# Optimization experiments

Hardware: AMD Instinct MI355X
Metric: run time of the kernel (lower is better)

Reference implementation:

```python
import jax, jax.numpy as jnp
import numpy as np

HEADS = 2
K_HOP = 2
RATIO = 0.8
NEG_SLOPE = 0.01


def seg_softmax(logits, seg, num_seg):
    # torch_geometric.utils.softmax: numerically stable segment softmax
    m = jax.ops.segment_max(logits, seg, num_segments=num_seg)
    e = jnp.exp(logits - m[seg])
    d = jax.ops.segment_sum(e, seg, num_segments=num_seg)
    return e / d[seg]


def _attention(key_value, query, seg, num_seg, Wk, W1, W2, W3):
    # Attention.forward with enable_BN=False; weights stored [in,out] so x@W == torch Linear
    a = key_value @ Wk
    h = jnp.concatenate([a, query, a - query, a * query], axis=-1)  # [N,4H]
    h = jax.nn.leaky_relu(h @ W1, NEG_SLOPE)
    h = jax.nn.leaky_relu(h @ W2, NEG_SLOPE)
    h = jax.nn.leaky_relu(h @ W3, NEG_SLOPE)  # [N,1]
    return seg_softmax(h[:, 0], seg, num_seg)[:, None]  # att_weights [N,1]


def setup_inputs():
    key = jax.random.key(0)
    ks = jax.random.split(key, 10)
    B, n, H, epg = 64, 64, 128, 2048
    N = B * n
    x = jax.random.normal(ks[0], (N, H), jnp.float32)
    src = jax.random.randint(ks[1], (B, epg), 0, n)
    dst = jax.random.randint(ks[2], (B, epg), 0, n)
    off = (jnp.arange(B) * n)[:, None]
    edge_index = jnp.stack([(src + off).reshape(-1), (dst + off).reshape(-1)], 0)
    edge_weight = jax.random.uniform(ks[3], (B * epg,), jnp.float32)
    target_x = jax.random.normal(ks[4], (B, H), jnp.float32)
    batch_ixs = jnp.repeat(jnp.arange(B), n)
    s = lambda i, sh: jax.random.normal(ks[i], sh, jnp.float32) / np.sqrt(sh[-2])
    # index 0=cluster_att, 1=query_att, 2=cluster_att2, 3=query_att2
    att_Wk = s(5, (4, H, H))
    att_W1 = s(6, (4, 4 * H, 2 * H))
    att_W2 = s(7, (4, 2 * H, H))
    att_W3 = s(8, (4, H, 1))
    lin_W = s(9, (HEADS, H, H))
    return dict(x=x, edge_index=edge_index, edge_weight=edge_weight, target_x=target_x,
                batch_ixs=batch_ixs, att_Wk=att_Wk, att_W1=att_W1, att_W2=att_W2,
                att_W3=att_W3, lin_W=lin_W)


def reference(x, edge_index, edge_weight, target_x, batch_ixs, att_Wk, att_W1, att_W2, att_W3, lin_W):
    N, H = x.shape
    B = target_x.shape[0]
    n = N // B
    # ---- gcn_norm with self loops (fill 1.0) ----
    loop = jnp.arange(N)
    row = jnp.concatenate([edge_index[0], loop])
    col = jnp.concatenate([edge_index[1], loop])
    w = jnp.concatenate([edge_weight, jnp.ones((N,), edge_weight.dtype)])
    deg = jax.ops.segment_sum(w, col, num_segments=N)
    dinv = jnp.where(deg > 0, jax.lax.rsqrt(jnp.maximum(deg, 1e-12)), 0.0)
    ew = dinv[row] * w * dinv[col]  # [L]
    # ---- k-hop propagation ----
    def hop(v):
        return jax.ops.segment_sum(v[row] * ew[:, None], col, num_segments=N)
    x_q = x
    for _ in range(K_HOP):
        x_q = hop(x_q)
    qt = target_x[batch_ixs]  # repeat_interleave by per-graph counts (sorted batch)
    # ---- multi-head edge attention (reuse_att_w=True, dropout=0 -> E identical per head) ----
    f1 = _attention(x, x_q, batch_ixs, B, att_Wk[0], att_W1[0], att_W2[0], att_W3[0])
    f2 = _attention(x, qt, batch_ixs, B, att_Wk[1], att_W1[1], att_W2[1], att_W3[1])
    E = jax.nn.leaky_relu(f1[col] + f2[row], NEG_SLOPE)  # [L,1]
    E = seg_softmax(E[:, 0], col, N)[:, None]
    x_c = jnp.zeros_like(x)
    E_g = jnp.zeros((row.shape[0], 1), x.dtype)
    agg = jax.ops.segment_sum(x[row] * E, col, num_segments=N)
    for h in range(HEADS):
        x_c = x_c + jax.nn.leaky_relu(x + agg @ lin_W[h], NEG_SLOPE)
        E_g = E_g + E
    x_c = x_c / HEADS
    E_g = E_g / HEADS
    # ---- second k-hop + cluster scoring ----
    x_q2 = x_c
    for _ in range(K_HOP):
        x_q2 = hop(x_q2)
    g1 = _attention(x_c, x_q2, batch_ixs, B, att_Wk[2], att_W1[2], att_W2[2], att_W3[2])
    g2 = _attention(x_c, qt, batch_ixs, B, att_Wk[3], att_W1[3], att_W2[3], att_W3[3])
    # stack over heads then mean == g1+g2 (same attention modules reused per head)
    cluster_score = seg_softmax((g1 + g2)[:, 0], batch_ixs, B)  # [N]
    # ---- per-graph topk (ratio) ----
    kk = int(np.ceil(RATIO * n))
    _, idx = jax.lax.top_k(cluster_score.reshape(B, n), kk)  # descending, matches PyG topk
    perm = (idx + (jnp.arange(B) * n)[:, None]).reshape(-1)  # [Nk]
    x_out = x[perm] * cluster_score[perm][:, None]
    batch_out = batch_ixs[perm]
    # ---- S^T A S (dense equivalent of SparseTensor triple product) ----
    A_d = jnp.zeros((N, N), x.dtype).at[row, col].add(ew)
    S_d = jnp.zeros((N, N), x.dtype).at[row, col].add(E_g[:, 0])
    S_p = S_d[:, perm]  # S[:, perm] -> [N, Nk]
    A2 = S_p.T @ (A_d @ S_p)  # [Nk, Nk]
    Nk = perm.shape[0]
    A2 = A2.at[jnp.arange(Nk), jnp.arange(Nk)].set(1.0)  # fill_diag(1.0)
    return x_out, A2, batch_out, perm
```

## Files before the change

### kernel.cpp

```cpp
#include <hip/hip_runtime.h>

#define KK 52
#define NKOUT 3328
#define NEG 0.01f

typedef __attribute__((ext_vector_type(8))) __bf16 bf16x8;
typedef __attribute__((ext_vector_type(16))) float floatx16;

__device__ __forceinline__ float lrelu(float v){ return v > 0.f ? v : NEG*v; }

#define SW(r, ko) ((r)*40 + ((ko) ^ ((((r)>>3)&3) << 3)))

__device__ __forceinline__ void split_store8(const float* vv, __bf16* P0, __bf16* P1, __bf16* P2, int addr){
  bf16x8 p1, p2, p3;
  #pragma unroll
  for (int j = 0; j < 8; j++){
    __bf16 b1 = (__bf16)vv[j];
    float r1 = vv[j] - (float)b1;
    __bf16 b2 = (__bf16)r1;
    float r2 = r1 - (float)b2;
    p1[j] = b1; p2[j] = b2; p3[j] = (__bf16)r2;
  }
  *(bf16x8*)(P0 + addr) = p1;
  *(bf16x8*)(P1 + addr) = p2;
  *(bf16x8*)(P2 + addr) = p3;
}

__device__ __forceinline__ void mfma6(const __bf16* A0, const __bf16* A1, const __bf16* A2,
                                      const __bf16* B0, const __bf16* B1, const __bf16* B2,
                                      int aoff, int boff, floatx16* acc){
  bf16x8 a1 = *(const bf16x8*)(A0 + aoff);
  bf16x8 a2 = *(const bf16x8*)(A1 + aoff);
  bf16x8 a3 = *(const bf16x8*)(A2 + aoff);
  bf16x8 b1 = *(const bf16x8*)(B0 + boff);
  bf16x8 b2 = *(const bf16x8*)(B1 + boff);
  bf16x8 b3 = *(const bf16x8*)(B2 + boff);
  floatx16 c = *acc;
  c = __builtin_amdgcn_mfma_f32_32x32x16_bf16(a1,b1,c,0,0,0);
  c = __builtin_amdgcn_mfma_f32_32x32x16_bf16(a1,b2,c,0,0,0);
  c = __builtin_amdgcn_mfma_f32_32x32x16_bf16(a2,b1,c,0,0,0);
  c = __builtin_amdgcn_mfma_f32_32x32x16_bf16(a1,b3,c,0,0,0);
  c = __builtin_amdgcn_mfma_f32_32x32x16_bf16(a3,b1,c,0,0,0);
  c = __builtin_amdgcn_mfma_f32_32x32x16_bf16(a2,b2,c,0,0,0);
  *acc = c;
}

__device__ __forceinline__ void g_gemm(const float* __restrict__ A0, int ldA,
                                       const float* __restrict__ W0, int ldW, int K,
                                       __bf16* pb, floatx16* oA, floatx16* oB){
  __bf16 *As0 = pb, *As1 = pb+2560, *As2 = pb+5120;
  __bf16 *Bs0 = pb+7680, *Bs1 = pb+12800, *Bs2 = pb+17920;
  int tid = threadIdx.x;
  int sar = tid >> 2, sako = (tid & 3)*8;
  int bn = tid & 127, bk = (tid >> 7)*16;
  int wv_ = tid >> 6, L = tid & 63, m = L & 31, half = L >> 5;
  int rA = 32*(wv_ & 1) + m, rB0 = (wv_ >> 1)*32 + m, rB1 = rB0 + 64;
  const float* arow = A0 + (size_t)sar*ldA;
  floatx16 accA, accB;
  #pragma unroll
  for (int i = 0; i < 16; i++){ accA[i] = 0.f; accB[i] = 0.f; }
  float ra[8], wv[16];
  {
    float4 v0 = *(const float4*)(arow + sako);
    float4 v1 = *(const float4*)(arow + sako + 4);
    ra[0]=v0.x; ra[1]=v0.y; ra[2]=v0.z; ra[3]=v0.w; ra[4]=v1.x; ra[5]=v1.y; ra[6]=v1.z; ra[7]=v1.w;
    #pragma unroll
    for (int j = 0; j < 16; j++) wv[j] = W0[(size_t)(bk + j)*ldW + bn];
  }
  for (int k0 = 0; k0 < K; k0 += 32){
    split_store8(ra, As0, As1, As2, SW(sar, sako));
    split_store8(wv,     Bs0, Bs1, Bs2, SW(bn, bk));
    split_store8(wv + 8, Bs0, Bs1, Bs2, SW(bn, bk + 8));
    __syncthreads();
    int k1 = k0 + 32;
    float ra2[8], wv2[16];
    if (k1 < K){
      float4 v0 = *(const float4*)(arow + k1 + sako);
      float4 v1 = *(const float4*)(arow + k1 + sako + 4);
      ra2[0]=v0.x; ra2[1]=v0.y; ra2[2]=v0.z; ra2[3]=v0.w; ra2[4]=v1.x; ra2[5]=v1.y; ra2[6]=v1.z; ra2[7]=v1.w;
      #pragma unroll
      for (int j = 0; j < 16; j++) wv2[j] = W0[(size_t)(k1 + bk + j)*ldW + bn];
    }
    #pragma unroll
    for (int kg = 0; kg < 2; kg++){
      int ko = kg*16 + half*8;
      mfma6(As0,As1,As2, Bs0,Bs1,Bs2, SW(rA,ko), SW(rB0,ko), &accA);
      mfma6(As0,As1,As2, Bs0,Bs1,Bs2, SW(rA,ko), SW(rB1,ko), &accB);
    }
    __syncthreads();
    if (k1 < K){
      #pragma unroll
      for (int j = 0; j < 8; j++) ra[j] = ra2[j];
      #pragma unroll
      for (int j = 0; j < 16; j++) wv[j] = wv2[j];
    }
  }
  *oA = accA; *oB = accB;
}

__device__ __forceinline__ void g_gemm64(const float* __restrict__ A0, int ldA,
                                         const float* __restrict__ W0, int ldW, int K,
                                         __bf16* pb, floatx16* oC){
  __bf16 *As0 = pb, *As1 = pb+2560, *As2 = pb+5120;
  __bf16 *Bs0 = pb+7680, *Bs1 = pb+10240, *Bs2 = pb+12800;
  int tid = threadIdx.x;
  int sar = tid >> 2, sako = (tid & 3)*8;
  int bn = tid & 63, bk = (tid >> 6)*8;
  int wv_ = tid >> 6, L = tid & 63, m = L & 31, half = L >> 5;
  int rA = 32*(wv_ & 1) + m, rB = 32*(wv_ >> 1) + m;
  const float* arow = A0 + (size_t)sar*ldA;
  floatx16 acc;
  #pragma unroll
  for (int i = 0; i < 16; i++) acc[i] = 0.f;
  float ra[8], wv[8];
  {
    float4 v0 = *(const float4*)(arow + sako);
    float4 v1 = *(const float4*)(arow + sako + 4);
    ra[0]=v0.x; ra[1]=v0.y; ra[2]=v0.z; ra[3]=v0.w; ra[4]=v1.x; ra[5]=v1.y; ra[6]=v1.z; ra[7]=v1.w;
    #pragma unroll
    for (int j = 0; j < 8; j++) wv[j] = W0[(size_t)(bk + j)*ldW + bn];
  }
  for (int k0 = 0; k0 < K; k0 += 32){
    split_store8(ra, As0, As1, As2, SW(sar, sako));
    split_store8(wv, Bs0, Bs1, Bs2, SW(bn, bk));
    __syncthreads();
    int k1 = k0 + 32;
    float ra2[8], wv2[8];
    if (k1 < K){
      float4 v0 = *(const float4*)(arow + k1 + sako);
      float4 v1 = *(const float4*)(arow + k1 + sako + 4);
      ra2[0]=v0.x; ra2[1]=v0.y; ra2[2]=v0.z; ra2[3]=v0.w; ra2[4]=v1.x; ra2[5]=v1.y; ra2[6]=v1.z; ra2[7]=v1.w;
      #pragma unroll
      for (int j = 0; j < 8; j++) wv2[j] = W0[(size_t)(k1 + bk + j)*ldW + bn];
    }
    #pragma unroll
    for (int kg = 0; kg < 2; kg++){
      int ko = kg*16 + half*8;
      mfma6(As0,As1,As2, Bs0,Bs1,Bs2, SW(rA,ko), SW(rB,ko), &acc);
    }
    __syncthreads();
    if (k1 < K){
      #pragma unroll
      for (int j = 0; j < 8; j++){ ra[j] = ra2[j]; wv[j] = wv2[j]; }
    }
  }
  *oC = acc;
}

__device__ __forceinline__ void g_gemm_h64(const float* __restrict__ arow, const float* __restrict__ qrow,
                                           const float* __restrict__ W1fz, int colbase,
                                           __bf16* pb, floatx16* oC){
  __bf16 *As0 = pb, *As1 = pb+2560, *As2 = pb+5120;
  __bf16 *Bs0 = pb+7680, *Bs1 = pb+10240, *Bs2 = pb+12800;
  int tid = threadIdx.x;
  int sar = tid >> 2, sako = (tid & 3)*8;
  int bn = tid & 63, bk = (tid >> 6)*8;
  int col = colbase + bn;
  int wv_ = tid >> 6, L = tid & 63, m = L & 31, half = L >> 5;
  int rA = 32*(wv_ & 1) + m, rB = 32*(wv_ >> 1) + m;
  auto loadA = [&](int k0, float* r){
    int seg = k0 >> 7, kl = (k0 & 127) + sako;
    if (seg == 0){
      float4 a0 = *(const float4*)(arow + kl), a1 = *(const float4*)(arow + kl + 4);
      r[0]=a0.x; r[1]=a0.y; r[2]=a0.z; r[3]=a0.w; r[4]=a1.x; r[5]=a1.y; r[6]=a1.z; r[7]=a1.w;
    } else if (seg == 1){
      float4 q0 = *(const float4*)(qrow + kl), q1 = *(const float4*)(qrow + kl + 4);
      r[0]=q0.x; r[1]=q0.y; r[2]=q0.z; r[3]=q0.w; r[4]=q1.x; r[5]=q1.y; r[6]=q1.z; r[7]=q1.w;
    } else {
      float4 a0 = *(const float4*)(arow + kl), a1 = *(const float4*)(arow + kl + 4);
      float4 q0 = *(const float4*)(qrow + kl), q1 = *(const float4*)(qrow + kl + 4);
      r[0]=a0.x*q0.x; r[1]=a0.y*q0.y; r[2]=a0.z*q0.z; r[3]=a0.w*q0.w;
      r[4]=a1.x*q1.x; r[5]=a1.y*q1.y; r[6]=a1.z*q1.z; r[7]=a1.w*q1.w;
    }
  };
  auto loadB = [&](int k0, float* r){
    #pragma unroll
    for (int j = 0; j < 8; j++) r[j] = W1fz[(size_t)(k0 + bk + j)*256 + col];
  };
  floatx16 acc;
  #pragma unroll
  for (int i = 0; i < 16; i++) acc[i] = 0.f;
  float ra[8], wv[8];
  loadA(0, ra); loadB(0, wv);
  for (int k0 = 0; k0 < 384; k0 += 32){
    split_store8(ra, As0, As1, As2, SW(sar, sako));
    split_store8(wv, Bs0, Bs1, Bs2, SW(bn, bk));
    __syncthreads();
    int k1 = k0 + 32;
    float ra2[8], wv2[8];
    if (k1 < 384){ loadA(k1, ra2); loadB(k1, wv2); }
    #pragma unroll
    for (int kg = 0; kg < 2; kg++){
      int ko = kg*16 + half*8;
      mfma6(As0,As1,As2, Bs0,Bs1,Bs2, SW(rA,ko), SW(rB,ko), &acc);
    }
    __syncthreads();
    if (k1 < 384){
      #pragma unroll
      for (int j = 0; j < 8; j++){ ra[j] = ra2[j]; wv[j] = wv2[j]; }
    }
  }
  *oC = acc;
}

__device__ __forceinline__ void c_write(floatx16 accA, floatx16 accB, float* C0, int ldC, int act){
  int tid = threadIdx.x, wv_ = tid >> 6, L = tid & 63, m = L & 31, half = L >> 5;
  int rB0 = (wv_ >> 1)*32 + m, rB1 = rB0 + 64;
  int row0 = 32*(wv_ & 1) + 4*half;
  #pragma unroll
  for (int reg = 0; reg < 16; reg++){
    int row = row0 + (reg & 3) + 8*(reg >> 2);
    float va = accA[reg], vb = accB[reg];
    if (act){ va = lrelu(va); vb = lrelu(vb); }
    C0[(size_t)row*ldC + rB0] = va;
    C0[(size_t)row*ldC + rB1] = vb;
  }
}

__device__ __forceinline__ void c_write64(floatx16 acc, float* C0, int ldC, int act){
  int tid = threadIdx.x, wv_ = tid >> 6, L = tid & 63, m = L & 31, half = L >> 5;
  int col = 32*(wv_ >> 1) + m;
  int row0 = 32*(wv_ & 1) + 4*half;
  #pragma unroll
  for (int reg = 0; reg < 16; reg++){
    int row = row0 + (reg & 3) + 8*(reg >> 2);
    float v = acc[reg];
    if (act) v = lrelu(v);
    C0[(size_t)row*ldC + col] = v;
  }
}

__device__ __forceinline__ void hop2_run(const float* A, const float* VfullL,
                                         const float* srcG, float* dstG,
                                         float* Vt, float* Tt){
  int tid = threadIdx.x;
  int tc = (tid & 31)*2, tf = (tid >> 5)*4;
  for (int f0 = 0; f0 < 128; f0 += 32){
    if (!VfullL){
      for (int o = tid; o < 2048; o += 256){
        int r = o >> 5, f = o & 31;
        Vt[o] = srcG[r*128 + f0 + f];
      }
      __syncthreads();
    }
    float a00,a01,a02,a03,a10,a11,a12,a13;
    a00=a01=a02=a03=a10=a11=a12=a13=0.f;
    for (int r = 0; r < 64; r++){
      float x0 = A[r*64 + tc], x1 = A[r*64 + tc + 1];
      float4 v4 = VfullL ? *(const float4*)&VfullL[r*128 + f0 + tf]
                         : *(const float4*)&Vt[r*32 + tf];
      a00 += x0*v4.x; a01 += x0*v4.y; a02 += x0*v4.z; a03 += x0*v4.w;
      a10 += x1*v4.x; a11 += x1*v4.y; a12 += x1*v4.z; a13 += x1*v4.w;
    }
    *(float4*)&Tt[tc*32 + tf]     = make_float4(a00,a01,a02,a03);
    *(float4*)&Tt[(tc+1)*32 + tf] = make_float4(a10,a11,a12,a13);
    __syncthreads();
    a00=a01=a02=a03=a10=a11=a12=a13=0.f;
    for (int r = 0; r < 64; r++){
      float x0 = A[r*64 + tc], x1 = A[r*64 + tc + 1];
      float4 v4 = *(const float4*)&Tt[r*32 + tf];
      a00 += x0*v4.x; a01 += x0*v4.y; a02 += x0*v4.z; a03 += x0*v4.w;
      a10 += x1*v4.x; a11 += x1*v4.y; a12 += x1*v4.z; a13 += x1*v4.w;
    }
    *(float4*)(dstG + tc*128 + f0 + tf)     = make_float4(a00,a01,a02,a03);
    *(float4*)(dstG + (tc+1)*128 + f0 + tf) = make_float4(a10,a11,a12,a13);
    __syncthreads();
  }
}

__global__ __launch_bounds__(256) void k_p0(const int* __restrict__ ei, const float* __restrict__ ew,
                                            const float* __restrict__ x, const float* __restrict__ Wk,
                                            const float* __restrict__ W1,
                                            float* A_g, float* M_g, float* xq, float* a_buf, float* W1f,
                                            float* outA2){
  __shared__ __align__(16) char POOL[57856];
  float* pf = (float*)POOL;
  __bf16* pb = (__bf16*)POOL;
  int blk = blockIdx.x, tid = threadIdx.x;
  if (blk < 64){
    int b = blk;
    float* Ws = pf; float* Mc = pf + 4096; float* dv = pf + 8192;
    for (int i = tid; i < 4096; i += 256){ Ws[i] = 0.f; Mc[i] = 0.f; }
    __syncthreads();
    const int* r0 = ei + b*2048;
    const int* c0 = ei + 64*2048 + b*2048;
    const float* w0 = ew + b*2048;
    int base = b*64;
    for (int e = tid; e < 2048; e += 256){
      int r = r0[e] - base, c = c0[e] - base;
      atomicAdd(&Ws[r*64 + c], w0[e]);
      atomicAdd(&Mc[r*64 + c], 1.f);
    }
    if (tid < 64){ atomicAdd(&Ws[tid*65], 1.f); atomicAdd(&Mc[tid*65], 1.f); }
    __syncthreads();
    if (tid < 64){
      float d = 0.f;
      for (int r = 0; r < 64; r++) d += Ws[r*64 + tid];
      dv[tid] = d > 0.f ? rsqrtf(fmaxf(d, 1e-12f)) : 0.f;
    }
    __syncthreads();
    for (int i = tid; i < 4096; i += 256){
      int r = i >> 6, c = i & 63;
      float a = dv[r]*Ws[i]*dv[c];
      Ws[i] = a;
      A_g[b*4096 + i] = a;
      M_g[b*4096 + i] = Mc[i];
    }
    __syncthreads();
    hop2_run(Ws, nullptr, x + (size_t)b*8192, xq + (size_t)b*8192, pf + 8256, pf + 10304);
  } else if (blk < 192){
    int idx = blk - 64, z = idx >> 6, b = idx & 63;
    floatx16 cA, cB;
    g_gemm(x + (size_t)b*8192, 128, Wk + (size_t)z*16384, 128, 128, pb, &cA, &cB);
    c_write(cA, cB, a_buf + (size_t)z*524288 + (size_t)b*8192, 128, 0);
  } else if (blk < 256){
    int idx0 = (blk - 192)*6144;
    for (int i = tid; i < 6144; i += 256){
      int g = idx0 + i;
      int zz = g / 98304;
      int r = g - zz*98304;
      int kr = r >> 8, c = r & 255;
      const float* Wz = W1 + (size_t)zz*131072;
      float v;
      if (kr < 128)       v = Wz[kr*256 + c] + Wz[(kr + 256)*256 + c];
      else if (kr < 256)  v = Wz[kr*256 + c] - Wz[(kr + 128)*256 + c];
      else                v = Wz[(kr + 128)*256 + c];
      W1f[g] = v;
    }
  } else {
    float4* p = (float4*)outA2;
    int base = (blk - 256)*1024 + tid;
    #pragma unroll
    for (int i = 0; i < 4; i++) p[base + i*256] = make_float4(0.f,0.f,0.f,0.f);
  }
}

__global__ __launch_bounds__(256) void k_h1(const float* __restrict__ a_buf, const float* __restrict__ q0,
                                            const float* __restrict__ tgt, const float* __restrict__ W1fp,
                                            float* h1){
  __shared__ __align__(16) char POOL[30720];
  __bf16* pb = (__bf16*)POOL;
  int blk = blockIdx.x, tid = threadIdx.x;
  int b = blk >> 3, z = (blk >> 2) & 1, nq = blk & 3;
  int sar = tid >> 2;
  const float* arow = a_buf + (size_t)z*524288 + ((size_t)b*64 + sar)*128;
  const float* qrow = z ? (tgt + (size_t)b*128) : (q0 + ((size_t)b*64 + sar)*128);
  floatx16 c;
  g_gemm_h64(arow, qrow, W1fp + (size_t)z*98304, nq*64, pb, &c);
  c_write64(c, h1 + (size_t)z*1048576 + (size_t)b*16384 + nq*64, 256, 1);
}

__global__ __launch_bounds__(256) void k_w2p(const float* __restrict__ h1, const float* __restrict__ W2,
                                             const float* __restrict__ W3, float* __restrict__ lp){
  __shared__ __align__(16) char POOL[30720];
  __shared__ float lgp[128];
  __bf16* pb = (__bf16*)POOL;
  int blk = blockIdx.x, tid = threadIdx.x;
  int b = blk >> 2, z = (blk >> 1) & 1, nh = blk & 1;
  floatx16 c;
  g_gemm64(h1 + (size_t)z*1048576 + (size_t)b*16384, 256,
           W2 + (size_t)z*32768 + nh*64, 128, 256, pb, &c);
  int wv_ = tid >> 6, L = tid & 63, m = L & 31, half = L >> 5;
  int col = 32*(wv_ >> 1) + m;
  float w = W3[z*128 + nh*64 + col];
  float v[16];
  #pragma unroll
  for (int reg = 0; reg < 16; reg++) v[reg] = lrelu(c[reg])*w;
  #pragma unroll
  for (int off = 1; off < 32; off <<= 1)
    #pragma unroll
    for (int reg = 0; reg < 16; reg++) v[reg] += __shfl_xor(v[reg], off);
  if (m == 0){
    #pragma unroll
    for (int reg = 0; reg < 16; reg++) lgp[wv_*32 + half*16 + reg] = v[reg];
  }
  __syncthreads();
  if (tid < 64){
    int row = tid, rh = row >> 5, rem = row & 31;
    int hf = (rem >> 2) & 1, rg = (rem & 3) + 4*(rem >> 3);
    float p = lgp[rh*32 + hf*16 + rg] + lgp[(rh + 2)*32 + hf*16 + rg];
    lp[(z*2 + nh)*4096 + b*64 + row] = p;
  }
}

__global__ __launch_bounds__(256) void k_edge(const float* __restrict__ M_g, const float* __restrict__ lp,
                                              const float* __restrict__ x, float* __restrict__ S_g,
                                              float* __restrict__ agg){
  __shared__ __align__(16) float Mc[4096];
  __shared__ __align__(16) float xb[8192];
  __shared__ float f1s[64], f2s[64];
  int b = blockIdx.x, tid = threadIdx.x;
  for (int i = tid; i < 4096; i += 256) Mc[i] = M_g[b*4096 + i];
  for (int i = tid*4; i < 8192; i += 1024)
    *(float4*)&xb[i] = *(const float4*)(x + (size_t)b*8192 + i);
  if (tid < 128){
    int z = tid >> 6, r = tid & 63;
    float d = lp[(z*2)*4096 + b*64 + r] + lp[(z*2 + 1)*4096 + b*64 + r];
    float l = lrelu(d);
    float mx = l;
    #pragma unroll
    for (int off = 32; off; off >>= 1) mx = fmaxf(mx, __shfl_xor(mx, off));
    float e = expf(l - mx);
    float s = e;
    #pragma unroll
    for (int off = 32; off; off >>= 1) s += __shfl_xor(s, off);
    (z ? f2s : f1s)[r] = e/s;
  }
  __syncthreads();
  int c = tid >> 2, sub = tid & 3;
  float m = -1e30f;
  for (int r = sub; r < 64; r += 4)
    if (Mc[r*64 + c] > 0.f) m = fmaxf(m, lrelu(f1s[c] + f2s[r]));
  m = fmaxf(m, __shfl_xor(m, 1));
  m = fmaxf(m, __shfl_xor(m, 2));
  float s = 0.f;
  for (int r = sub; r < 64; r += 4){
    float mc = Mc[r*64 + c];
    if (mc > 0.f) s += mc*expf(lrelu(f1s[c] + f2s[r]) - m);
  }
  s += __shfl_xor(s, 1);
  s += __shfl_xor(s, 2);
  for (int r = sub; r < 64; r += 4){
    float mc = Mc[r*64 + c];
    float v = 0.f;
    if (mc > 0.f) v = mc*expf(lrelu(f1s[c] + f2s[r]) - m)/s;
    Mc[r*64 + c] = v;
  }
  __syncthreads();
  for (int i = tid; i < 4096; i += 256) S_g[b*4096 + i] = Mc[i];
  int tc = (tid & 15)*4, tf = (tid >> 4)*8;
  float acc[4][8];
  #pragma unroll
  for (int i = 0; i < 4; i++)
    #pragma unroll
    for (int j = 0; j < 8; j++) acc[i][j] = 0.f;
  for (int r = 0; r < 64; r++){
    float4 e4 = *(const float4*)&Mc[r*64 + tc];
    float4 x0 = *(const float4*)&xb[r*128 + tf];
    float4 x1 = *(const float4*)&xb[r*128 + tf + 4];
    float e_[4] = {e4.x,e4.y,e4.z,e4.w};
    float x_[8] = {x0.x,x0.y,x0.z,x0.w,x1.x,x1.y,x1.z,x1.w};
    #pragma unroll
    for (int ci = 0; ci < 4; ci++)
      #pragma unroll
      for (int fj = 0; fj < 8; fj++) acc[ci][fj] += e_[ci]*x_[fj];
  }
  #pragma unroll
  for (int ci = 0; ci < 4; ci++){
    *(float4*)(agg + (size_t)b*8192 + (tc+ci)*128 + tf)     = make_float4(acc[ci][0],acc[ci][1],acc[ci][2],acc[ci][3]);
    *(float4*)(agg + (size_t)b*8192 + (tc+ci)*128 + tf + 4) = make_float4(acc[ci][4],acc[ci][5],acc[ci][6],acc[ci][7]);
  }
}

__global__ __launch_bounds__(256) void k_linxchop(const float* __restrict__ aggb, const float* __restrict__ x,
                                                  const float* __restrict__ linW, const float* __restrict__ A_g,
                                                  float* xcb, float* xq2){
  __shared__ __align__(16) char POOL[57856];
  float* pf = (float*)POOL;
  __bf16* pb = (__bf16*)POOL;
  int b = blockIdx.x, tid = threadIdx.x;
  floatx16 h0A, h0B, h1A, h1B2;
  g_gemm(aggb + (size_t)b*8192, 128, linW, 128, 128, pb, &h0A, &h0B);
  g_gemm(aggb + (size_t)b*8192, 128, linW + 16384, 128, 128, pb, &h1A, &h1B2);
  float* xcV = pf; float* Ab = pf + 8192; float* Tt = pf + 12288;
  {
    int wv_ = tid >> 6, L = tid & 63, m = L & 31, half = L >> 5;
    int rB0 = (wv_ >> 1)*32 + m, rB1 = rB0 + 64, row0 = 32*(wv_ & 1) + 4*half;
    #pragma unroll
    for (int reg = 0; reg < 16; reg++){
      int row = row0 + (reg & 3) + 8*(reg >> 2);
      float xv0 = x[((size_t)b*64 + row)*128 + rB0];
      float v0 = 0.5f*(lrelu(xv0 + h0A[reg]) + lrelu(xv0 + h1A[reg]));
      xcV[row*128 + rB0] = v0;
      xcb[(size_t)b*8192 + row*128 + rB0] = v0;
      float xv1 = x[((size_t)b*64 + row)*128 + rB1];
      float v1 = 0.5f*(lrelu(xv1 + h0B[reg]) + lrelu(xv1 + h1B2[reg]));
      xcV[row*128 + rB1] = v1;
      xcb[(size_t)b*8192 + row*128 + rB1] = v1;
    }
  }
  for (int i = tid*4; i < 4096; i += 1024)
    *(float4*)&Ab[i] = *(const float4*)(A_g + b*4096 + i);
  __syncthreads();
  hop2_run(Ab, xcV, nullptr, xq2 + (size_t)b*8192, Tt, Tt);
}

__global__ __launch_bounds__(256) void k_wkg(const float* __restrict__ xcb, const float* __restrict__ Wkg,
                                             float* a_buf){
  __shared__ __align__(16) char POOL[30720];
  __bf16* pb = (__bf16*)POOL;
  int blk = blockIdx.x;
  int b = blk >> 2, z = (blk >> 1) & 1, nh = blk & 1;
  floatx16 c;
  g_gemm64(xcb + (size_t)b*8192, 128, Wkg + (size_t)z*16384 + nh*64, 128, 128, pb, &c);
  c_write64(c, a_buf + (size_t)z*524288 + (size_t)b*8192 + nh*64, 128, 0);
}

__global__ __launch_bounds__(256) void k_A2c(const float* __restrict__ lp, const float* __restrict__ x,
                                             const float* __restrict__ A_g, const float* __restrict__ S_g,
                                             float* outA2, float* outX, float* outB, float* outP){
  __shared__ __align__(16) float At[64*68];
  __shared__ __align__(16) float Sp[64*56];
  __shared__ __align__(16) float Tq[64*56];
  __shared__ int pi[64];
  __shared__ float pv[64];
  int b = blockIdx.x, tid = threadIdx.x;
  if (tid < 64){
    int lane = tid;
    float f[2];
    #pragma unroll
    for (int z = 0; z < 2; z++){
      float d = lp[(z*2)*4096 + b*64 + lane] + lp[(z*2 + 1)*4096 + b*64 + lane];
      float l = lrelu(d);
      float mx = l;
      #pragma unroll
      for (int off = 32; off; off >>= 1) mx = fmaxf(mx, __shfl_xor(mx, off));
      float e = expf(l - mx);
      float sm = e;
      #pragma unroll
      for (int off = 32; off; off >>= 1) sm += __shfl_xor(sm, off);
      f[z] = e/sm;
    }
    float l = f[0] + f[1];
    float m = l;
    #pragma unroll
    for (int off = 32; off; off >>= 1) m = fmaxf(m, __shfl_xor(m, off));
    float e = expf(l - m);
    float sm = e;
    #pragma unroll
    for (int off = 32; off; off >>= 1) sm += __shfl_xor(sm, off);
    float v = e/sm;
    int idx = lane;
    #pragma unroll
    for (int k = 2; k <= 64; k <<= 1){
      #pragma unroll
      for (int j = k >> 1; j > 0; j >>= 1){
        float ov = __shfl_xor(v, j);
        int   oi = __shfl_xor(idx, j);
        bool ascBlock = (lane & k) == 0;
        bool iAmLow   = (lane & j) == 0;
        bool otherPrec = (ov > v) || (ov == v && oi < idx);
        bool take = (ascBlock == iAmLow) ? otherPrec : !otherPrec;
        if (take){ v = ov; idx = oi; }
      }
    }
    pi[lane] = idx; pv[lane] = v;
    if (lane < KK){
      outB[b*KK + lane] = (float)b;
      outP[b*KK + lane] = (float)(b*64 + idx);
    }
  }
  __syncthreads();
  for (int o = tid*4; o < KK*128; o += 1024){
    int j = o >> 7, f = o & 127;
    float4 xv = *(const float4*)(x + ((size_t)b*64 + pi[j])*128 + f);
    float sv = pv[j];
    *(float4*)(outX + (size_t)b*KK*128 + o) = make_float4(xv.x*sv, xv.y*sv, xv.z*sv, xv.w*sv);
  }
  for (int idx = tid; idx < 4096; idx += 256){
    int i = idx >> 6, k = idx & 63;
    At[k*68 + i] = A_g[b*4096 + idx];
  }
  for (int idx = tid; idx < 4096; idx += 256){
    int k = idx >> 6, t = idx & 63;
    if (t < 56) Sp[k*56 + t] = (t < KK) ? S_g[b*4096 + k*64 + pi[t]] : 0.f;
  }
  __syncthreads();
  if (tid < 224){
    int i0 = (tid/14)*4, t0 = (tid % 14)*4;
    float acc[4][4];
    #pragma unroll
    for (int a = 0; a < 4; a++)
      #pragma unroll
      for (int c = 0; c < 4; c++) acc[a][c] = 0.f;
    for (int k = 0; k < 64; k++){
      float4 a4 = *(const float4*)&At[k*68 + i0];
      float4 s4 = *(const float4*)&Sp[k*56 + t0];
      float a_[4] = {a4.x,a4.y,a4.z,a4.w};
      float s_[4] = {s4.x,s4.y,s4.z,s4.w};
      #pragma unroll
      for (int ii = 0; ii < 4; ii++)
        #pragma unroll
        for (int tt = 0; tt < 4; tt++) acc[ii][tt] += a_[ii]*s_[tt];
    }
    #pragma unroll
    for (int ii = 0; ii < 4; ii++)
      *(float4*)&Tq[(i0+ii)*56 + t0] = make_float4(acc[ii][0],acc[ii][1],acc[ii][2],acc[ii][3]);
  }
  __syncthreads();
  if (tid < 169){
    int a0 = (tid/13)*4, t0 = (tid % 13)*4;
    float acc[4][4];
    #pragma unroll
    for (int a = 0; a < 4; a++)
      #pragma unroll
      for (int c = 0; c < 4; c++) acc[a][c] = 0.f;
    for (int i = 0; i < 64; i++){
      float4 s4 = *(const float4*)&Sp[i*56 + a0];
      float4 t4 = *(const float4*)&Tq[i*56 + t0];
      float s_[4] = {s4.x,s4.y,s4.z,s4.w};
      float t_[4] = {t4.x,t4.y,t4.z,t4.w};
      #pragma unroll
      for (int aa = 0; aa < 4; aa++)
        #pragma unroll
        for (int tt = 0; tt < 4; tt++) acc[aa][tt] += s_[aa]*t_[tt];
    }
    #pragma unroll
    for (int aa = 0; aa < 4; aa++){
      int a = a0 + aa;
      float4 o;
      o.x = (a == t0    ) ? 1.f : acc[aa][0];
      o.y = (a == t0 + 1) ? 1.f : acc[aa][1];
      o.z = (a == t0 + 2) ? 1.f : acc[aa][2];
      o.w = (a == t0 + 3) ? 1.f : acc[aa][3];
      *(float4*)(outA2 + (size_t)(b*KK + a)*NKOUT + b*KK + t0) = o;
    }
  }
}

extern "C" void kernel_launch(void* const* d_in, const int* in_sizes, int n_in,
                              void* d_out, int out_size, void* d_ws, size_t ws_size,
                              hipStream_t stream){
  const float* x    = (const float*)d_in[0];
  const int*   ei   = (const int*)d_in[1];
  const float* ew   = (const float*)d_in[2];
  const float* tgt  = (const float*)d_in[3];
  const float* Wk   = (const float*)d_in[5];
  const float* W1   = (const float*)d_in[6];
  const float* W2   = (const float*)d_in[7];
  const float* W3   = (const float*)d_in[8];
  const float* linW = (const float*)d_in[9];
  float* out = (float*)d_out;

  float* wf   = (float*)d_ws;
  float* A_g  = wf;
  float* M_g  = wf + 262144;
  float* S_g  = wf + 524288;
  float* xq   = wf + 786432;
  float* xq2  = wf + 1310720;
  float* aggb = wf + 1835008;
  float* xcb  = wf + 2359296;
  float* a_buf= wf + 2883584;
  float* h1   = wf + 3932160;
  float* lp   = wf + 6029312;
  float* W1f  = wf + 6045696;

  float* outX  = out;
  float* outA2 = out + 425984;
  float* outB  = out + 425984 + 11075584;
  float* outP  = outB + NKOUT;

  k_p0<<<dim3(2960), dim3(256), 0, stream>>>(ei, ew, x, Wk, W1, A_g, M_g, xq, a_buf, W1f, outA2);
  k_h1<<<dim3(512), dim3(256), 0, stream>>>(a_buf, xq, tgt, W1f, h1);
  k_w2p<<<dim3(256), dim3(256), 0, stream>>>(h1, W2, W3, lp);
  k_edge<<<dim3(64), dim3(256), 0, stream>>>(M_g, lp, x, S_g, aggb);
  k_linxchop<<<dim3(64), dim3(256), 0, stream>>>(aggb, x, linW, A_g, xcb, xq2);
  k_wkg<<<dim3(256), dim3(256), 0, stream>>>(xcb, Wk + 2*16384, a_buf);
  k_h1<<<dim3(512), dim3(256), 0, stream>>>(a_buf, xq2, tgt, W1f + 2*98304, h1);
  k_w2p<<<dim3(256), dim3(256), 0, stream>>>(h1, W2 + 2*32768, W3 + 2*128, lp);
  k_A2c<<<dim3(64), dim3(256), 0, stream>>>(lp, x, A_g, S_g, outA2, outX, outB, outP);
}
```

Measured before the change: 241.3 us.

## Fuse edge softmax aggregation with linear+hop kernel; split first hop across feature halves

The edge-attention aggregation kernel and the linear/k-hop kernel are merged into one kernel that keeps the aggregated features and x tile in a larger shared-memory pool, removing a global round-trip for agg and one launch. Separately, the first k-hop in k_p0 is split into two blocks per graph, each handling half of the feature columns, so more blocks run in parallel at the cost of duplicating the adjacency build. The fused kernel uses about 128KB of shared memory, which limits occupancy to one block per CU, but it only runs 64 blocks anyway.

New measurement: 227.8 us. 1.06x faster.

```diff
diff --git a/kernel.cpp b/kernel.cpp
--- a/kernel.cpp
+++ b/kernel.cpp
@@ -45,7 +45,7 @@
   *acc = c;
 }
 
-__device__ __forceinline__ void g_gemm(const float* __restrict__ A0, int ldA,
+__device__ __forceinline__ void g_gemm(const float* A0, int ldA,
                                        const float* __restrict__ W0, int ldW, int K,
                                        __bf16* pb, floatx16* oA, floatx16* oB){
   __bf16 *As0 = pb, *As1 = pb+2560, *As2 = pb+5120;
@@ -232,10 +232,10 @@
 
 __device__ __forceinline__ void hop2_run(const float* A, const float* VfullL,
                                          const float* srcG, float* dstG,
-                                         float* Vt, float* Tt){
+                                         float* Vt, float* Tt, int fbeg, int fend){
   int tid = threadIdx.x;
   int tc = (tid & 31)*2, tf = (tid >> 5)*4;
-  for (int f0 = 0; f0 < 128; f0 += 32){
+  for (int f0 = fbeg; f0 < fend; f0 += 32){
     if (!VfullL){
       for (int o = tid; o < 2048; o += 256){
         int r = o >> 5, f = o & 31;
@@ -277,8 +277,8 @@
   float* pf = (float*)POOL;
   __bf16* pb = (__bf16*)POOL;
   int blk = blockIdx.x, tid = threadIdx.x;
-  if (blk < 64){
-    int b = blk;
+  if (blk < 128){
+    int b = blk >> 1, fh = blk & 1;
     float* Ws = pf; float* Mc = pf + 4096; float* dv = pf + 8192;
     for (int i = tid; i < 4096; i += 256){ Ws[i] = 0.f; Mc[i] = 0.f; }
     __syncthreads();
@@ -303,18 +303,21 @@
       int r = i >> 6, c = i & 63;
       float a = dv[r]*Ws[i]*dv[c];
       Ws[i] = a;
-      A_g[b*4096 + i] = a;
-      M_g[b*4096 + i] = Mc[i];
-    }
-    __syncthreads();
-    hop2_run(Ws, nullptr, x + (size_t)b*8192, xq + (size_t)b*8192, pf + 8256, pf + 10304);
-  } else if (blk < 192){
-    int idx = blk - 64, z = idx >> 6, b = idx & 63;
+      if (fh == 0){
+        A_g[b*4096 + i] = a;
+        M_g[b*4096 + i] = Mc[i];
+      }
+    }
+    __syncthreads();
+    hop2_run(Ws, nullptr, x + (size_t)b*8192, xq + (size_t)b*8192, pf + 8256, pf + 10304,
+             fh*64, fh*64 + 64);
+  } else if (blk < 256){
+    int idx = blk - 128, z = idx >> 6, b = idx & 63;
     floatx16 cA, cB;
     g_gemm(x + (size_t)b*8192, 128, Wk + (size_t)z*16384, 128, 128, pb, &cA, &cB);
     c_write(cA, cB, a_buf + (size_t)z*524288 + (size_t)b*8192, 128, 0);
-  } else if (blk < 256){
-    int idx0 = (blk - 192)*6144;
+  } else if (blk < 320){
+    int idx0 = (blk - 256)*6144;
     for (int i = tid; i < 6144; i += 256){
       int g = idx0 + i;
       int zz = g / 98304;
@@ -329,7 +332,7 @@
     }
   } else {
     float4* p = (float4*)outA2;
-    int base = (blk - 256)*1024 + tid;
+    int base = (blk - 320)*1024 + tid;
     #pragma unroll
     for (int i = 0; i < 4; i++) p[base + i*256] = make_float4(0.f,0.f,0.f,0.f);
   }
@@ -383,12 +386,17 @@
   }
 }
 
-__global__ __launch_bounds__(256) void k_edge(const float* __restrict__ M_g, const float* __restrict__ lp,
-                                              const float* __restrict__ x, float* __restrict__ S_g,
-                                              float* __restrict__ agg){
-  __shared__ __align__(16) float Mc[4096];
-  __shared__ __align__(16) float xb[8192];
-  __shared__ float f1s[64], f2s[64];
+__global__ __launch_bounds__(256) void k_edgelin(const float* __restrict__ M_g, const float* __restrict__ lp,
+                                                 const float* __restrict__ x, const float* __restrict__ linW,
+                                                 const float* __restrict__ A_g,
+                                                 float* S_g, float* xcb, float* xq2){
+  __shared__ __align__(16) char POOL[128512];
+  __bf16* pb = (__bf16*)POOL;
+  float* f1s = (float*)(POOL + 46080);
+  float* f2s = (float*)(POOL + 46336);
+  float* Mc  = (float*)(POOL + 46592);
+  float* xb  = (float*)(POOL + 62976);
+  float* aggL= (float*)(POOL + 95744);
   int b = blockIdx.x, tid = threadIdx.x;
   for (int i = tid; i < 4096; i += 256) Mc[i] = M_g[b*4096 + i];
   for (int i = tid*4; i < 8192; i += 1024)
@@ -407,82 +415,79 @@
     (z ? f2s : f1s)[r] = e/s;
   }
   __syncthreads();
-  int c = tid >> 2, sub = tid & 3;
-  float m = -1e30f;
-  for (int r = sub; r < 64; r += 4)
-    if (Mc[r*64 + c] > 0.f) m = fmaxf(m, lrelu(f1s[c] + f2s[r]));
-  m = fmaxf(m, __shfl_xor(m, 1));
-  m = fmaxf(m, __shfl_xor(m, 2));
-  float s = 0.f;
-  for (int r = sub; r < 64; r += 4){
-    float mc = Mc[r*64 + c];
-    if (mc > 0.f) s += mc*expf(lrelu(f1s[c] + f2s[r]) - m);
-  }
-  s += __shfl_xor(s, 1);
-  s += __shfl_xor(s, 2);
-  for (int r = sub; r < 64; r += 4){
-    float mc = Mc[r*64 + c];
-    float v = 0.f;
-    if (mc > 0.f) v = mc*expf(lrelu(f1s[c] + f2s[r]) - m)/s;
-    Mc[r*64 + c] = v;
+  {
+    int c = tid >> 2, sub = tid & 3;
+    float m = -1e30f;
+    for (int r = sub; r < 64; r += 4)
+      if (Mc[r*64 + c] > 0.f) m = fmaxf(m, lrelu(f1s[c] + f2s[r]));
+    m = fmaxf(m, __shfl_xor(m, 1));
+    m = fmaxf(m, __shfl_xor(m, 2));
+    float s = 0.f;
+    for (int r = sub; r < 64; r += 4){
+      float mc = Mc[r*64 + c];
+      if (mc > 0.f) s += mc*expf(lrelu(f1s[c] + f2s[r]) - m);
+    }
+    s += __shfl_xor(s, 1);
+    s += __shfl_xor(s, 2);
+    for (int r = sub; r < 64; r += 4){
+      float mc = Mc[r*64 + c];
+      float v = 0.f;
+      if (mc > 0.f) v = mc*expf(lrelu(f1s[c] + f2s[r]) - m)/s;
+      Mc[r*64 + c] = v;
+    }
   }
   __syncthreads();
   for (int i = tid; i < 4096; i += 256) S_g[b*4096 + i] = Mc[i];
-  int tc = (tid & 15)*4, tf = (tid >> 4)*8;
-  float acc[4][8];
-  #pragma unroll
-  for (int i = 0; i < 4; i++)
-    #pragma unroll
-    for (int j = 0; j < 8; j++) acc[i][j] = 0.f;
-  for (int r = 0; r < 64; r++){
-    float4 e4 = *(const float4*)&Mc[r*64 + tc];
-    float4 x0 = *(const float4*)&xb[r*128 + tf];
-    float4 x1 = *(const float4*)&xb[r*128 + tf + 4];
-    float e_[4] = {e4.x,e4.y,e4.z,e4.w};
-    float x_[8] = {x0.x,x0.y,x0.z,x0.w,x1.x,x1.y,x1.z,x1.w};
-    #pragma unroll
-    for (int ci = 0; ci < 4; ci++)
-      #pragma unroll
-      for (int fj = 0; fj < 8; fj++) acc[ci][fj] += e_[ci]*x_[fj];
-  }
-  #pragma unroll
-  for (int ci = 0; ci < 4; ci++){
-    *(float4*)(agg + (size_t)b*8192 + (tc+ci)*128 + tf)     = make_float4(acc[ci][0],acc[ci][1],acc[ci][2],acc[ci][3]);
-    *(float4*)(agg + (size_t)b*8192 + (tc+ci)*128 + tf + 4) = make_float4(acc[ci][4],acc[ci][5],acc[ci][6],acc[ci][7]);
-  }
-}
-
-__global__ __launch_bounds__(256) void k_linxchop(const float* __restrict__ aggb, const float* __restrict__ x,
-                                                  const float* __restrict__ linW, const float* __restrict__ A_g,
-                                                  float* xcb, float* xq2){
-  __shared__ __align__(16) char POOL[57856];
-  float* pf = (float*)POOL;
-  __bf16* pb = (__bf16*)POOL;
-  int b = blockIdx.x, tid = threadIdx.x;
+  {
+    int tc = (tid & 15)*4, tf = (tid >> 4)*8;
+    float acc[4][8];
+    #pragma unroll
+    for (int i = 0; i < 4; i++)
+      #pragma unroll
+      for (int j = 0; j < 8; j++) acc[i][j] = 0.f;
+    for (int r = 0; r < 64; r++){
+      float4 e4 = *(const float4*)&Mc[r*64 + tc];
+      float4 x0 = *(const float4*)&xb[r*128 + tf];
+      float4 x1 = *(const float4*)&xb[r*128 + tf + 4];
+      float e_[4] = {e4.x,e4.y,e4.z,e4.w};
+      float x_[8] = {x0.x,x0.y,x0.z,x0.w,x1.x,x1.y,x1.z,x1.w};
+      #pragma unroll
+      for (int ci = 0; ci < 4; ci++)
+        #pragma unroll
+        for (int fj = 0; fj < 8; fj++) acc[ci][fj] += e_[ci]*x_[fj];
+    }
+    #pragma unroll
+    for (int ci = 0; ci < 4; ci++){
+      *(float4*)&aggL[(tc+ci)*128 + tf]     = make_float4(acc[ci][0],acc[ci][1],acc[ci][2],acc[ci][3]);
+      *(float4*)&aggL[(tc+ci)*128 + tf + 4] = make_float4(acc[ci][4],acc[ci][5],acc[ci][6],acc[ci][7]);
+    }
+  }
+  __syncthreads();
   floatx16 h0A, h0B, h1A, h1B2;
-  g_gemm(aggb + (size_t)b*8192, 128, linW, 128, 128, pb, &h0A, &h0B);
-  g_gemm(aggb + (size_t)b*8192, 128, linW + 16384, 128, 128, pb, &h1A, &h1B2);
-  float* xcV = pf; float* Ab = pf + 8192; float* Tt = pf + 12288;
+  g_gemm(aggL, 128, linW, 128, 128, pb, &h0A, &h0B);
+  g_gemm(aggL, 128, linW + 16384, 128, 128, pb, &h1A, &h1B2);
   {
     int wv_ = tid >> 6, L = tid & 63, m = L & 31, half = L >> 5;
     int rB0 = (wv_ >> 1)*32 + m, rB1 = rB0 + 64, row0 = 32*(wv_ & 1) + 4*half;
     #pragma unroll
     for (int reg = 0; reg < 16; reg++){
       int row = row0 + (reg & 3) + 8*(reg >> 2);
-      float xv0 = x[((size_t)b*64 + row)*128 + rB0];
+      float xv0 = xb[row*128 + rB0];
       float v0 = 0.5f*(lrelu(xv0 + h0A[reg]) + lrelu(xv0 + h1A[reg]));
-      xcV[row*128 + rB0] = v0;
+      xb[row*128 + rB0] = v0;
       xcb[(size_t)b*8192 + row*128 + rB0] = v0;
-      float xv1 = x[((size_t)b*64 + row)*128 + rB1];
+      float xv1 = xb[row*128 + rB1];
       float v1 = 0.5f*(lrelu(xv1 + h0B[reg]) + lrelu(xv1 + h1B2[reg]));
-      xcV[row*128 + rB1] = v1;
+      xb[row*128 + rB1] = v1;
       xcb[(size_t)b*8192 + row*128 + rB1] = v1;
     }
   }
+  float* Ab = (float*)POOL;
+  float* Tt = (float*)(POOL + 16384);
   for (int i = tid*4; i < 4096; i += 1024)
     *(float4*)&Ab[i] = *(const float4*)(A_g + b*4096 + i);
   __syncthreads();
-  hop2_run(Ab, xcV, nullptr, xq2 + (size_t)b*8192, Tt, Tt);
+  hop2_run(Ab, xb, nullptr, xq2 + (size_t)b*8192, Tt, Tt, 0, 128);
 }
 
 __global__ __launch_bounds__(256) void k_wkg(const float* __restrict__ xcb, const float* __restrict__ Wkg,
@@ -638,7 +643,6 @@
   float* S_g  = wf + 524288;
   float* xq   = wf + 786432;
   float* xq2  = wf + 1310720;
-  float* aggb = wf + 1835008;
   float* xcb  = wf + 2359296;
   float* a_buf= wf + 2883584;
   float* h1   = wf + 3932160;
@@ -650,11 +654,10 @@
   float* outB  = out + 425984 + 11075584;
   float* outP  = outB + NKOUT;
 
-  k_p0<<<dim3(2960), dim3(256), 0, stream>>>(ei, ew, x, Wk, W1, A_g, M_g, xq, a_buf, W1f, outA2);
+  k_p0<<<dim3(3024), dim3(256), 0, stream>>>(ei, ew, x, Wk, W1, A_g, M_g, xq, a_buf, W1f, outA2);
   k_h1<<<dim3(512), dim3(256), 0, stream>>>(a_buf, xq, tgt, W1f, h1);
   k_w2p<<<dim3(256), dim3(256), 0, stream>>>(h1, W2, W3, lp);
-  k_edge<<<dim3(64), dim3(256), 0, stream>>>(M_g, lp, x, S_g, aggb);
-  k_linxchop<<<dim3(64), dim3(256), 0, stream>>>(aggb, x, linW, A_g, xcb, xq2);
+  k_edgelin<<<dim3(64), dim3(256), 0, stream>>>(M_g, lp, x, linW, A_g, S_g, xcb, xq2);
   k_wkg<<<dim3(256), dim3(256), 0, stream>>>(xcb, Wk + 2*16384, a_buf);
   k_h1<<<dim3(512), dim3(256), 0, stream>>>(a_buf, xq2, tgt, W1f + 2*98304, h1);
   k_w2p<<<dim3(256), dim3(256), 0, stream>>>(h1, W2 + 2*32768, W3 + 2*128, lp);
```
